# Kernel tuning notes

Hardware: AMD Instinct MI355X
Metric: run time of the kernel (lower is better)

## Reference

```python
import jax, jax.numpy as jnp
import numpy as np

D, H, L = 88, 256, 128  # input_dim, hidden_dim, latent_dim
B, T = 128, 1024


def setup_inputs() -> dict:
    key = jax.random.key(0)
    ks = jax.random.split(key, 16)
    s = 1.0 / np.sqrt(H)
    u = lambda k, shape: jax.random.uniform(k, shape, jnp.float32, -s, s)
    return {
        "x": jax.random.uniform(ks[0], (B, T, D), jnp.float32),  # piano-roll in [0,1)
        "Wih_e": u(ks[1], (4 * H, D)),
        "Whh_e": u(ks[2], (4 * H, H)),
        "bih_e": u(ks[3], (4 * H,)),
        "bhh_e": u(ks[4], (4 * H,)),
        "Wih_d": u(ks[5], (4 * H, D)),
        "Whh_d": u(ks[6], (4 * H, H)),
        "bih_d": u(ks[7], (4 * H,)),
        "bhh_d": u(ks[8], (4 * H,)),
        "W_lat": u(ks[9], (L, H)),
        "b_lat": u(ks[10], (L,)),
        "W_decinit": u(ks[11], (H, L)),
        "b_decinit": u(ks[12], (H,)),
        "W_out": u(ks[13], (D, H)),
        "b_out": u(ks[14], (D,)),
    }


def _lstm_cell(x_t, h, c, Wih, Whh, b):
    # PyTorch gate order: i, f, g, o
    gates = x_t @ Wih.T + h @ Whh.T + b  # [B, 4H]
    i, f, g, o = jnp.split(gates, 4, axis=-1)
    c_new = jax.nn.sigmoid(f) * c + jax.nn.sigmoid(i) * jnp.tanh(g)
    h_new = jax.nn.sigmoid(o) * jnp.tanh(c_new)
    return h_new, c_new


def reference(x, Wih_e, Whh_e, bih_e, bhh_e, Wih_d, Whh_d, bih_d, bhh_d,
              W_lat, b_lat, W_decinit, b_decinit, W_out, b_out):
    batch, seq_len, _ = x.shape
    b_e = bih_e + bhh_e
    b_d = bih_d + bhh_d

    # ---- encoder LSTM: scan over time, keep final hidden state ----
    def enc_step(carry, x_t):
        h, c = carry
        h, c = _lstm_cell(x_t, h, c, Wih_e, Whh_e, b_e)
        return (h, c), None

    h0 = jnp.zeros((batch, H), x.dtype)
    (h_n, _), _ = jax.lax.scan(enc_step, (h0, h0), jnp.swapaxes(x, 0, 1))

    # ---- latent + decoder init ----
    z = h_n @ W_lat.T + b_lat                     # [B, L]
    h_dec0 = z @ W_decinit.T + b_decinit          # [B, H]
    c_dec0 = jnp.zeros_like(h_dec0)
    inp0 = jnp.zeros((batch, D), x.dtype)

    def dec_step(carry, _):
        h, c, inp = carry
        h, c = _lstm_cell(inp, h, c, Wih_d, Whh_d, b_d)
        pred = jax.nn.sigmoid(h @ W_out.T + b_out)  # [B, D]
        return (h, c, pred), pred

    _, preds = jax.lax.scan(dec_step, (h_dec0, c_dec0, inp0), None, length=seq_len)
    outputs = jnp.swapaxes(preds, 0, 1)           # [B, T, D]
    return outputs, z
```

## Files before the change

kernel.cpp:

```cpp
#include <hip/hip_runtime.h>


typedef unsigned int u32;
typedef unsigned long long u64;
typedef unsigned short u16;

typedef _Float16 v8h __attribute__((ext_vector_type(8)));
typedef float    v4f __attribute__((ext_vector_type(4)));
typedef u32      v4u __attribute__((ext_vector_type(4)));

union H8 { v8h v; u64 q[2]; v4u u4; u32 d[4]; _Float16 h[8]; u16 s[8]; };

#define ENC_TAG(t) (0x4000u + (u32)(t))
#define DEC_TAG(t) (0x4800u + (u32)(t))
#define XW_OFF_U32   65536ull
#define XW_U32_PER_G 786432ull
#define WS_NEED ((XW_OFF_U32 + 8ull*XW_U32_PER_G) * 4ull)

static __device__ __forceinline__ float fsig(float x){
  return __builtin_amdgcn_rcpf(1.f + __builtin_amdgcn_exp2f(-1.4426950408889634f*x));
}
static __device__ __forceinline__ float ftanh(float x){
  return 1.f - 2.f*__builtin_amdgcn_rcpf(1.f + __builtin_amdgcn_exp2f(2.8853900817779268f*x));
}
static __device__ __forceinline__ u32 f2tag(float f, u32 tag){
  union{ _Float16 h; u16 b; } u; u.h = (_Float16)f;
  return (tag << 16) | (u32)u.b;
}

static __device__ __forceinline__ void st_pk4(u32* p, v4u val){
  asm volatile("global_store_dwordx4 %0, %1, off sc0 sc1" :: "v"(p), "v"(val) : "memory");
}
static __device__ __forceinline__ void poll_issue(const u32* p, v4u& q){
  asm volatile("global_load_dwordx4 %0, %1, off sc0 sc1" : "=v"(q) : "v"(p) : "memory");
}
static __device__ __forceinline__ void poll_sc01(const u32* p, v4u& q){
  asm volatile("global_load_dwordx4 %0, %1, off sc0 sc1\n\ts_waitcnt vmcnt(0)"
               : "=v"(q) : "v"(p) : "memory");
}
static __device__ __forceinline__ void poll_wait(v4u& q){
  asm volatile("s_waitcnt vmcnt(0)" : "+v"(q) :: "memory");
}

static __device__ __forceinline__ void poll_finish(const u32* p, u32 tag, v4u& q,
                                                   _Float16* dstbuf, int rbase, int scol){
  const u32 tm = tag << 16;
  poll_wait(q);
  u32 it = 0;
  for(;;){
    u32 bad = (q[0]^tm)|(q[1]^tm)|(q[2]^tm)|(q[3]^tm);
    if (__all((bad & 0xFFFF0000u) == 0)) break;
    if ((++it & 15u) == 0u) __builtin_amdgcn_s_sleep(1);
    poll_sc01(p, q);
  }
  #pragma unroll
  for (int j = 0; j < 4; ++j){
    const int row = rbase + j;
    const int ab = (row*512 + scol*2) ^ ((row&7)<<4);
    *(u16*)((char*)dstbuf + ab) = (u16)(q[j] & 0xFFFFu);
  }
}

static __device__ __forceinline__ v4u frag_h(const _Float16* b, int row, int colh){
  const int a = (row*512 + colh*2) ^ ((row&7)<<4);
  return *(const v4u*)((const char*)b + a);
}
static __device__ __forceinline__ v4u frag_x(const _Float16* b, int row, int colh){
  const int a = (row*256 + colh*2) ^ ((row&7)<<4);
  return *(const v4u*)((const char*)b + a);
}

static __device__ __forceinline__ void build_Bw(v8h Bw[4][11], const float* Wih,
                                                const float* Whh, int wcol, int quad, int hf){
  #pragma unroll
  for (int nt = 0; nt < 4; ++nt){
    const int n = nt*256 + wcol;
    #pragma unroll
    for (int kt = 0; kt < 11; ++kt){
      H8 a;
      #pragma unroll
      for (int j = 0; j < 8; ++j){
        float val;
        if (kt < 3){
          const int k = kt*32 + quad*8 + j;
          val = (k < 88) ? Wih[n*88 + k] : 0.f;
        } else {
          const int base = (kt < 7) ? (hf*128 + (kt-3)*32) : ((1-hf)*128 + (kt-7)*32);
          val = Whh[n*256 + base + quad*8 + j];
        }
        a.h[j] = (_Float16)val;
      }
      Bw[nt][kt] = a.v;
    }
  }
}

template<bool XW>
static __device__ __forceinline__ void load_Ax(H8 Ax[3], const float* x, const u32* xwg,
                                               int g, int t, int c, int quad, int l){
  if constexpr (XW){
    const u32* xb = xwg + (u64)t*768ull;
    #pragma unroll
    for (int kt = 0; kt < 3; ++kt)
      Ax[kt].u4 = *(const v4u*)(xb + kt*256 + l*4);
  } else {
    const float* xb = x + ((u64)(g*16 + c)*1024ull + (u64)t)*88ull;
    #pragma unroll
    for (int kt = 0; kt < 3; ++kt){
      if (kt == 2 && quad == 3){ Ax[kt].q[0] = 0; Ax[kt].q[1] = 0; }
      else {
        const int k0 = kt*32 + quad*8;
        v4f f0 = *(const v4f*)(xb + k0);
        v4f f1 = *(const v4f*)(xb + k0 + 4);
        #pragma unroll
        for (int j = 0; j < 4; ++j){ Ax[kt].h[j] = (_Float16)f0[j]; Ax[kt].h[j+4] = (_Float16)f1[j]; }
      }
    }
  }
}

static __device__ __forceinline__ void emit_h(const v4f acc[4], const float bb[4], float cst[4],
                                              _Float16* dstbuf, u32* hx_slot, u32 tag,
                                              int c, int quad, int wcol){
  v4u pk;
  #pragma unroll
  for (int r = 0; r < 4; ++r){
    const float gi = acc[0][r] + bb[0];
    const float gf = acc[1][r] + bb[1];
    const float gg = acc[2][r] + bb[2];
    const float go = acc[3][r] + bb[3];
    const float cn = fsig(gf)*cst[r] + fsig(gi)*ftanh(gg);
    cst[r] = cn;
    const float hn = fsig(go)*ftanh(cn);
    const int row = quad*4 + r;
    const int ab = (row*512 + wcol*2) ^ ((row&7)<<4);
    *(_Float16*)((char*)dstbuf + ab) = (_Float16)hn;
    pk[r] = f2tag(hn, tag);
  }
  st_pk4(hx_slot + ((wcol & 127)*16 + quad*4), pk);
}

__global__ __launch_bounds__(256) void xconv(const float* __restrict__ x, u32* __restrict__ xw){
  const int flat = (int)blockIdx.x*256 + (int)threadIdx.x;
  const int l  = flat & 63;
  const int f2 = flat >> 6;
  const int kt = f2 % 3;
  const int f3 = f2 / 3;
  const int t  = f3 & 1023;
  const int g  = f3 >> 10;
  const int c = l & 15, quad = l >> 4;
  H8 a;
  if (kt == 2 && quad == 3){ a.q[0] = 0; a.q[1] = 0; }
  else {
    const float* xb = x + ((u64)(g*16 + c)*1024ull + (u64)t)*88ull + kt*32 + quad*8;
    v4f f0 = *(const v4f*)xb;
    v4f f1 = *(const v4f*)(xb + 4);
    #pragma unroll
    for (int j = 0; j < 4; ++j){ a.h[j] = (_Float16)f0[j]; a.h[j+4] = (_Float16)f1[j]; }
  }
  *(v4u*)(xw + (u64)flat*4ull) = a.u4;
}

template<bool XW>
__global__ __launch_bounds__(512, 2) void lstm_ae(
    const float* __restrict__ x,
    const float* __restrict__ Wih_e, const float* __restrict__ Whh_e,
    const float* __restrict__ bih_e, const float* __restrict__ bhh_e,
    const float* __restrict__ Wih_d, const float* __restrict__ Whh_d,
    const float* __restrict__ bih_d, const float* __restrict__ bhh_d,
    const float* __restrict__ W_lat, const float* __restrict__ b_lat,
    const float* __restrict__ W_decinit, const float* __restrict__ b_decinit,
    const float* __restrict__ W_out, const float* __restrict__ b_out,
    float* __restrict__ dout, char* __restrict__ ws)
{
  const int tid = (int)threadIdx.x;
  const int v = tid >> 6, l = tid & 63;
  const int c = l & 15, quad = l >> 4;
  const int bid = (int)blockIdx.x;
  const int g = bid & 7, hf = bid >> 3;
  const int wcol = hf*128 + v*16 + c;
  const int kL = hf*4;
  const int kR = 4 - hf*4;

  u32* wsu = (u32*)ws;
  u32* hx_w       = wsu + (u64)((g*2 + hf)*2)     * 2048ull;
  const u32* hx_r = wsu + (u64)((g*2 + (1-hf))*2) * 2048ull;
  const u32* xwg  = wsu + XW_OFF_U32 + (u64)g * XW_U32_PER_G;

  const int rbase = (tid & 3) * 4;
  const int scol  = (1-hf)*128 + (tid >> 2);

  __shared__ _Float16 h2[2][4096];
  __shared__ _Float16 xp[2048];
  __shared__ v4u woutlds[3072];

  #pragma unroll
  for (int i = 0; i < 6; ++i){
    const int fid = v*6 + i;
    const int nt = fid >> 3, kt = fid & 7;
    const int n = nt*16 + c, k0 = kt*32 + quad*8;
    H8 a;
    #pragma unroll
    for (int j = 0; j < 8; ++j)
      a.h[j] = (n < 88) ? (_Float16)W_out[n*256 + k0 + j] : (_Float16)0.f;
    woutlds[fid*64 + l] = a.u4;
  }

  v8h Bw[4][11];
  build_Bw(Bw, Wih_e, Whh_e, wcol, quad, hf);
  float bb[4];
  #pragma unroll
  for (int nt = 0; nt < 4; ++nt) bb[nt] = bih_e[nt*256 + wcol] + bhh_e[nt*256 + wcol];
  float cst[4] = {0.f, 0.f, 0.f, 0.f};
  __syncthreads();

  {
    H8 Ax[3];
    load_Ax<XW>(Ax, x, xwg, g, 0, c, quad, l);
    v4f acc[4];
    #pragma unroll
    for (int nt = 0; nt < 4; ++nt) acc[nt] = (v4f){0.f,0.f,0.f,0.f};
    #pragma unroll
    for (int kt = 0; kt < 3; ++kt)
      #pragma unroll
      for (int nt = 0; nt < 4; ++nt)
        acc[nt] = __builtin_amdgcn_mfma_f32_16x16x32_f16(Ax[kt].v, Bw[nt][kt], acc[nt], 0,0,0);
    emit_h(acc, bb, cst, h2[0], hx_w, ENC_TAG(0), c, quad, wcol);
    __syncthreads();
  }

  v4f accx[4];
  {
    H8 Ax[3];
    load_Ax<XW>(Ax, x, xwg, g, 1, c, quad, l);
    #pragma unroll
    for (int nt = 0; nt < 4; ++nt) accx[nt] = (v4f){0.f,0.f,0.f,0.f};
    #pragma unroll
    for (int kt = 0; kt < 3; ++kt)
      #pragma unroll
      for (int nt = 0; nt < 4; ++nt)
        accx[nt] = __builtin_amdgcn_mfma_f32_16x16x32_f16(Ax[kt].v, Bw[nt][kt], accx[nt], 0,0,0);
  }

  #pragma unroll 1
  for (int t = 1; t < 1024; ++t){
    const int cur = (t-1)&1, nxt = t&1;
    const u32* pp = hx_r + (u64)cur*2048ull + tid*4;
    v4u q; poll_issue(pp, q);

    v4f acc[4];
    #pragma unroll
    for (int nt = 0; nt < 4; ++nt) acc[nt] = accx[nt];

    H8 AhL[4];
    #pragma unroll
    for (int i = 0; i < 4; ++i) AhL[i].u4 = frag_h(h2[cur], c, (kL+i)*32 + quad*8);
    #pragma unroll
    for (int i = 0; i < 4; ++i)
      #pragma unroll
      for (int nt = 0; nt < 4; ++nt)
        acc[nt] = __builtin_amdgcn_mfma_f32_16x16x32_f16(AhL[i].v, Bw[nt][3+i], acc[nt], 0,0,0);

    if (t < 1023){
      H8 Ax[3];
      load_Ax<XW>(Ax, x, xwg, g, t+1, c, quad, l);
      #pragma unroll
      for (int nt = 0; nt < 4; ++nt) accx[nt] = (v4f){0.f,0.f,0.f,0.f};
      #pragma unroll
      for (int kt = 0; kt < 3; ++kt)
        #pragma unroll
        for (int nt = 0; nt < 4; ++nt)
          accx[nt] = __builtin_amdgcn_mfma_f32_16x16x32_f16(Ax[kt].v, Bw[nt][kt], accx[nt], 0,0,0);
    }

    poll_finish(pp, ENC_TAG(t-1), q, h2[cur], rbase, scol);
    __syncthreads();

    H8 AhR[4];
    #pragma unroll
    for (int i = 0; i < 4; ++i) AhR[i].u4 = frag_h(h2[cur], c, (kR+i)*32 + quad*8);
    #pragma unroll
    for (int i = 0; i < 4; ++i)
      #pragma unroll
      for (int nt = 0; nt < 4; ++nt)
        acc[nt] = __builtin_amdgcn_mfma_f32_16x16x32_f16(AhR[i].v, Bw[nt][7+i], acc[nt], 0,0,0);

    emit_h(acc, bb, cst, h2[nxt], hx_w + (u64)nxt*2048ull, ENC_TAG(t), c, quad, wcol);
    __syncthreads();
  }

  {
    const u32* pp = hx_r + 2048ull + tid*4;
    v4u q; poll_issue(pp, q);
    poll_finish(pp, ENC_TAG(1023), q, h2[1], rbase, scol);
    __syncthreads();
  }

  {
    H8 AhL[4], AhR[4];
    #pragma unroll
    for (int i = 0; i < 4; ++i) AhL[i].u4 = frag_h(h2[1], c, (kL+i)*32 + quad*8);
    #pragma unroll
    for (int i = 0; i < 4; ++i) AhR[i].u4 = frag_h(h2[1], c, (kR+i)*32 + quad*8);
    const int n = v*16 + c;
    v4f zacc = (v4f){0.f,0.f,0.f,0.f};
    #pragma unroll
    for (int i = 0; i < 4; ++i){
      H8 b; const int k0 = (kL+i)*32 + quad*8;
      #pragma unroll
      for (int j = 0; j < 8; ++j) b.h[j] = (_Float16)W_lat[n*256 + k0 + j];
      zacc = __builtin_amdgcn_mfma_f32_16x16x32_f16(AhL[i].v, b.v, zacc, 0,0,0);
    }
    #pragma unroll
    for (int i = 0; i < 4; ++i){
      H8 b; const int k0 = (kR+i)*32 + quad*8;
      #pragma unroll
      for (int j = 0; j < 8; ++j) b.h[j] = (_Float16)W_lat[n*256 + k0 + j];
      zacc = __builtin_amdgcn_mfma_f32_16x16x32_f16(AhR[i].v, b.v, zacc, 0,0,0);
    }
    const float bl = b_lat[n];
    #pragma unroll
    for (int r = 0; r < 4; ++r){
      const int m = quad*4 + r;
      const float zv = zacc[r] + bl;
      if (hf == 0)
        __builtin_nontemporal_store(zv, dout + 11534336ull + (u64)(g*16 + m)*128ull + n);
      const int ab = (m*256 + n*2) ^ ((m&7)<<4);
      *(_Float16*)((char*)xp + ab) = (_Float16)zv;
    }
    __syncthreads();
  }

  {
    H8 Az[4];
    #pragma unroll
    for (int kt = 0; kt < 4; ++kt) Az[kt].u4 = frag_x(xp, c, kt*32 + quad*8);
    #pragma unroll
    for (int half = 0; half < 2; ++half){
      const int n = half*128 + v*16 + c;
      v4f da = (v4f){0.f,0.f,0.f,0.f};
      #pragma unroll
      for (int kt = 0; kt < 4; ++kt){
        H8 b; const int k0 = kt*32 + quad*8;
        #pragma unroll
        for (int j = 0; j < 8; ++j) b.h[j] = (_Float16)W_decinit[n*128 + k0 + j];
        da = __builtin_amdgcn_mfma_f32_16x16x32_f16(Az[kt].v, b.v, da, 0,0,0);
      }
      const float bdi = b_decinit[n];
      #pragma unroll
      for (int r = 0; r < 4; ++r){
        const int row = quad*4 + r;
        const int ab = (row*512 + n*2) ^ ((row&7)<<4);
        *(_Float16*)((char*)h2[1] + ab) = (_Float16)(da[r] + bdi);
      }
    }
    __syncthreads();
  }

  build_Bw(Bw, Wih_d, Whh_d, wcol, quad, hf);
  #pragma unroll
  for (int nt = 0; nt < 4; ++nt) bb[nt] = bih_d[nt*256 + wcol] + bhh_d[nt*256 + wcol];
  float bo = 0.f;
  if (v < 6){ const int n = v*16 + c; bo = (n < 88) ? b_out[n] : 0.f; }
  #pragma unroll
  for (int r = 0; r < 4; ++r) cst[r] = 0.f;

  #pragma unroll 1
  for (int t = 0; t < 1024; ++t){
    const int cur = (t+1)&1, nxt = t&1;
    const u32* pp = hx_r + (u64)cur*2048ull + tid*4;
    v4u q;
    if (t > 0) poll_issue(pp, q);

    H8 AhL[4], AhR[4];
    v4f acc[4];
    #pragma unroll
    for (int nt = 0; nt < 4; ++nt) acc[nt] = (v4f){0.f,0.f,0.f,0.f};
    #pragma unroll
    for (int i = 0; i < 4; ++i) AhL[i].u4 = frag_h(h2[cur], c, (kL+i)*32 + quad*8);
    #pragma unroll
    for (int i = 0; i < 4; ++i)
      #pragma unroll
      for (int nt = 0; nt < 4; ++nt)
        acc[nt] = __builtin_amdgcn_mfma_f32_16x16x32_f16(AhL[i].v, Bw[nt][3+i], acc[nt], 0,0,0);

    v4f pacc = (v4f){0.f,0.f,0.f,0.f};
    if (t > 0 && v < 6){
      #pragma unroll
      for (int i = 0; i < 4; ++i){
        H8 b; b.u4 = woutlds[(v*8 + kL + i)*64 + l];
        pacc = __builtin_amdgcn_mfma_f32_16x16x32_f16(AhL[i].v, b.v, pacc, 0,0,0);
      }
    }

    if (t > 0) poll_finish(pp, DEC_TAG(t-1), q, h2[cur], rbase, scol);
    __syncthreads();

    #pragma unroll
    for (int i = 0; i < 4; ++i) AhR[i].u4 = frag_h(h2[cur], c, (kR+i)*32 + quad*8);
    #pragma unroll
    for (int i = 0; i < 4; ++i)
      #pragma unroll
      for (int nt = 0; nt < 4; ++nt)
        acc[nt] = __builtin_amdgcn_mfma_f32_16x16x32_f16(AhR[i].v, Bw[nt][7+i], acc[nt], 0,0,0);

    if (t > 0 && v < 6){
      #pragma unroll
      for (int i = 0; i < 4; ++i){
        H8 b; b.u4 = woutlds[(v*8 + kR + i)*64 + l];
        pacc = __builtin_amdgcn_mfma_f32_16x16x32_f16(AhR[i].v, b.v, pacc, 0,0,0);
      }
      const int n = v*16 + c;
      #pragma unroll
      for (int r = 0; r < 4; ++r){
        const float pv = fsig(pacc[r] + bo);
        const int m = quad*4 + r;
        const int ab = (m*256 + n*2) ^ ((m&7)<<4);
        *(_Float16*)((char*)xp + ab) = (_Float16)pv;
        if (hf == 0 && n < 88)
          __builtin_nontemporal_store(pv,
            dout + ((u64)(g*16 + m)*1024ull + (u64)(t-1))*88ull + n);
      }
    }
    __syncthreads();

    if (t > 0){
      H8 Ap[3];
      #pragma unroll
      for (int kt = 0; kt < 3; ++kt) Ap[kt].u4 = frag_x(xp, c, kt*32 + quad*8);
      #pragma unroll
      for (int kt = 0; kt < 3; ++kt)
        #pragma unroll
        for (int nt = 0; nt < 4; ++nt)
          acc[nt] = __builtin_amdgcn_mfma_f32_16x16x32_f16(Ap[kt].v, Bw[nt][kt], acc[nt], 0,0,0);
    }

    emit_h(acc, bb, cst, h2[nxt], hx_w + (u64)nxt*2048ull, DEC_TAG(t), c, quad, wcol);
    __syncthreads();
  }

  {
    const u32* pp = hx_r + 2048ull + tid*4;
    v4u q; poll_issue(pp, q);
    poll_finish(pp, DEC_TAG(1023), q, h2[1], rbase, scol);
    __syncthreads();
    if (hf == 0 && v < 6){
      const int n = v*16 + c;
      v4f pacc = (v4f){0.f,0.f,0.f,0.f};
      #pragma unroll
      for (int i = 0; i < 4; ++i){
        H8 a; a.u4 = frag_h(h2[1], c, (kL+i)*32 + quad*8);
        H8 b; b.u4 = woutlds[(v*8 + kL + i)*64 + l];
        pacc = __builtin_amdgcn_mfma_f32_16x16x32_f16(a.v, b.v, pacc, 0,0,0);
      }
      #pragma unroll
      for (int i = 0; i < 4; ++i){
        H8 a; a.u4 = frag_h(h2[1], c, (kR+i)*32 + quad*8);
        H8 b; b.u4 = woutlds[(v*8 + kR + i)*64 + l];
        pacc = __builtin_amdgcn_mfma_f32_16x16x32_f16(a.v, b.v, pacc, 0,0,0);
      }
      if (n < 88){
        #pragma unroll
        for (int r = 0; r < 4; ++r){
          const float pv = fsig(pacc[r] + bo);
          const int m = quad*4 + r;
          __builtin_nontemporal_store(pv,
            dout + ((u64)(g*16 + m)*1024ull + 1023ull)*88ull + n);
        }
      }
    }
  }
}

extern "C" void kernel_launch(void* const* d_in, const int* in_sizes, int n_in,
                              void* d_out, int out_size, void* d_ws, size_t ws_size,
                              hipStream_t stream){
  (void)in_sizes; (void)n_in; (void)out_size;
  const bool xw_ok = ws_size >= WS_NEED;
  if (xw_ok){
    hipLaunchKernelGGL(xconv, dim3(6144), dim3(256), 0, stream,
                       (const float*)d_in[0], (u32*)d_ws + XW_OFF_U32);
    hipLaunchKernelGGL((lstm_ae<true>), dim3(16), dim3(512), 0, stream,
      (const float*)d_in[0],  (const float*)d_in[1],  (const float*)d_in[2],
      (const float*)d_in[3],  (const float*)d_in[4],  (const float*)d_in[5],
      (const float*)d_in[6],  (const float*)d_in[7],  (const float*)d_in[8],
      (const float*)d_in[9],  (const float*)d_in[10], (const float*)d_in[11],
      (const float*)d_in[12], (const float*)d_in[13], (const float*)d_in[14],
      (float*)d_out, (char*)d_ws);
  } else {
    hipLaunchKernelGGL((lstm_ae<false>), dim3(16), dim3(512), 0, stream,
      (const float*)d_in[0],  (const float*)d_in[1],  (const float*)d_in[2],
      (const float*)d_in[3],  (const float*)d_in[4],  (const float*)d_in[5],
      (const float*)d_in[6],  (const float*)d_in[7],  (const float*)d_in[8],
      (const float*)d_in[9],  (const float*)d_in[10], (const float*)d_in[11],
      (const float*)d_in[12], (const float*)d_in[13], (const float*)d_in[14],
      (float*)d_out, (char*)d_ws);
  }
}
```

Baseline: 6.191 ms.

## Pair LSTM blocks by XCC and poll same-die partners with lighter cache scope

Each of the 16 blocks reads its XCC ID and publishes it to a control area that xconv zeroes. The blocks then agree on a pairing in which the two halves of a batch group run on the same XCC whenever possible. Paired blocks on the same die poll the exchanged hidden state with sc0-only loads, mostly skipping sc1, which is meant to cut the per-step cross-block handshake latency in both recurrences. This adds a startup rendezvous that assumes all 16 blocks are co-resident, and it relies on the L2 being coherent within an XCC.

```diff
diff --git a/kernel.cpp b/kernel.cpp
--- a/kernel.cpp
+++ b/kernel.cpp
@@ -15,7 +15,8 @@
 #define DEC_TAG(t) (0x4800u + (u32)(t))
 #define XW_OFF_U32   65536ull
 #define XW_U32_PER_G 786432ull
-#define WS_NEED ((XW_OFF_U32 + 8ull*XW_U32_PER_G) * 4ull)
+#define CTRL_OFF_U32 (XW_OFF_U32 + 8ull*XW_U32_PER_G)
+#define WS_NEED ((CTRL_OFF_U32 + 64ull) * 4ull)
 
 static __device__ __forceinline__ float fsig(float x){
   return __builtin_amdgcn_rcpf(1.f + __builtin_amdgcn_exp2f(-1.4426950408889634f*x));
@@ -31,10 +32,15 @@
 static __device__ __forceinline__ void st_pk4(u32* p, v4u val){
   asm volatile("global_store_dwordx4 %0, %1, off sc0 sc1" :: "v"(p), "v"(val) : "memory");
 }
-static __device__ __forceinline__ void poll_issue(const u32* p, v4u& q){
-  asm volatile("global_load_dwordx4 %0, %1, off sc0 sc1" : "=v"(q) : "v"(p) : "memory");
-}
-static __device__ __forceinline__ void poll_sc01(const u32* p, v4u& q){
+static __device__ __forceinline__ void poll_issue(const u32* p, v4u& q, bool same){
+  if (same) asm volatile("global_load_dwordx4 %0, %1, off sc0" : "=v"(q) : "v"(p) : "memory");
+  else      asm volatile("global_load_dwordx4 %0, %1, off sc0 sc1" : "=v"(q) : "v"(p) : "memory");
+}
+static __device__ __forceinline__ void poll_fast(const u32* p, v4u& q){
+  asm volatile("global_load_dwordx4 %0, %1, off sc0\n\ts_waitcnt vmcnt(0)"
+               : "=v"(q) : "v"(p) : "memory");
+}
+static __device__ __forceinline__ void poll_mall(const u32* p, v4u& q){
   asm volatile("global_load_dwordx4 %0, %1, off sc0 sc1\n\ts_waitcnt vmcnt(0)"
                : "=v"(q) : "v"(p) : "memory");
 }
@@ -43,15 +49,18 @@
 }
 
 static __device__ __forceinline__ void poll_finish(const u32* p, u32 tag, v4u& q,
-                                                   _Float16* dstbuf, int rbase, int scol){
+                                                   _Float16* dstbuf, int rbase, int scol,
+                                                   bool same){
   const u32 tm = tag << 16;
   poll_wait(q);
   u32 it = 0;
   for(;;){
     u32 bad = (q[0]^tm)|(q[1]^tm)|(q[2]^tm)|(q[3]^tm);
     if (__all((bad & 0xFFFF0000u) == 0)) break;
-    if ((++it & 15u) == 0u) __builtin_amdgcn_s_sleep(1);
-    poll_sc01(p, q);
+    ++it;
+    if ((it & 15u) == 0u) __builtin_amdgcn_s_sleep(1);
+    if (same && (it & 3u) != 0u) poll_fast(p, q);
+    else                         poll_mall(p, q);
   }
   #pragma unroll
   for (int j = 0; j < 4; ++j){
@@ -140,7 +149,11 @@
   st_pk4(hx_slot + ((wcol & 127)*16 + quad*4), pk);
 }
 
-__global__ __launch_bounds__(256) void xconv(const float* __restrict__ x, u32* __restrict__ xw){
+__global__ __launch_bounds__(256) void xconv(const float* __restrict__ x, u32* __restrict__ wsu){
+  if (blockIdx.x == 0 && threadIdx.x < 64)
+    __hip_atomic_store(&wsu[CTRL_OFF_U32 + threadIdx.x], 0u,
+                       __ATOMIC_RELAXED, __HIP_MEMORY_SCOPE_AGENT);
+  u32* xw = wsu + XW_OFF_U32;
   const int flat = (int)blockIdx.x*256 + (int)threadIdx.x;
   const int l  = flat & 63;
   const int f2 = flat >> 6;
@@ -177,12 +190,65 @@
   const int v = tid >> 6, l = tid & 63;
   const int c = l & 15, quad = l >> 4;
   const int bid = (int)blockIdx.x;
-  const int g = bid & 7, hf = bid >> 3;
+
+  u32* wsu = (u32*)ws;
+
+  __shared__ int pinfo[3];
+  if constexpr (XW){
+    if (tid == 0){
+      u32 xcc;
+      asm volatile("s_getreg_b32 %0, hwreg(HW_REG_XCC_ID)" : "=s"(xcc));
+      xcc &= 15u;
+      u32* ctrl = wsu + CTRL_OFF_U32;
+      __hip_atomic_store(&ctrl[8+bid], xcc + 1u, __ATOMIC_RELEASE, __HIP_MEMORY_SCOPE_AGENT);
+      int xs[16];
+      #pragma unroll 1
+      for(;;){
+        bool all = true;
+        #pragma unroll 1
+        for (int i = 0; i < 16; ++i){
+          const u32 vi = __hip_atomic_load(&ctrl[8+i], __ATOMIC_ACQUIRE, __HIP_MEMORY_SCOPE_AGENT);
+          xs[i] = (int)vi - 1;
+          all = all && (vi != 0u);
+        }
+        if (all) break;
+        __builtin_amdgcn_s_sleep(2);
+      }
+      int G = -1, HF = 0, SM = 0, pc = 0;
+      int lo[16]; int nl = 0;
+      #pragma unroll 1
+      for (int xc = 0; xc < 16; ++xc){
+        int prev = -1;
+        #pragma unroll 1
+        for (int i = 0; i < 16; ++i) if (xs[i] == xc){
+          if (prev < 0) prev = i;
+          else {
+            if (prev == bid){ G = pc; HF = 0; SM = 1; }
+            if (i    == bid){ G = pc; HF = 1; SM = 1; }
+            ++pc; prev = -1;
+          }
+        }
+        if (prev >= 0) lo[nl++] = prev;
+      }
+      #pragma unroll 1
+      for (int j = 0; j + 1 < nl; j += 2){
+        if (lo[j]   == bid){ G = pc; HF = 0; SM = 0; }
+        if (lo[j+1] == bid){ G = pc; HF = 1; SM = 0; }
+        ++pc;
+      }
+      if (G < 0){ G = bid & 7; HF = bid >> 3; SM = 0; }
+      pinfo[0] = G; pinfo[1] = HF; pinfo[2] = SM;
+    }
+    __syncthreads();
+  }
+  const int g    = XW ? pinfo[0] : (bid & 7);
+  const int hf   = XW ? pinfo[1] : (bid >> 3);
+  const bool same = XW ? (pinfo[2] != 0) : false;
+
   const int wcol = hf*128 + v*16 + c;
   const int kL = hf*4;
   const int kR = 4 - hf*4;
 
-  u32* wsu = (u32*)ws;
   u32* hx_w       = wsu + (u64)((g*2 + hf)*2)     * 2048ull;
   const u32* hx_r = wsu + (u64)((g*2 + (1-hf))*2) * 2048ull;
   const u32* xwg  = wsu + XW_OFF_U32 + (u64)g * XW_U32_PER_G;
@@ -246,7 +312,7 @@
   for (int t = 1; t < 1024; ++t){
     const int cur = (t-1)&1, nxt = t&1;
     const u32* pp = hx_r + (u64)cur*2048ull + tid*4;
-    v4u q; poll_issue(pp, q);
+    v4u q; poll_issue(pp, q, same);
 
     v4f acc[4];
     #pragma unroll
@@ -273,7 +339,7 @@
           accx[nt] = __builtin_amdgcn_mfma_f32_16x16x32_f16(Ax[kt].v, Bw[nt][kt], accx[nt], 0,0,0);
     }
 
-    poll_finish(pp, ENC_TAG(t-1), q, h2[cur], rbase, scol);
+    poll_finish(pp, ENC_TAG(t-1), q, h2[cur], rbase, scol, same);
     __syncthreads();
 
     H8 AhR[4];
@@ -291,8 +357,8 @@
 
   {
     const u32* pp = hx_r + 2048ull + tid*4;
-    v4u q; poll_issue(pp, q);
-    poll_finish(pp, ENC_TAG(1023), q, h2[1], rbase, scol);
+    v4u q; poll_issue(pp, q, same);
+    poll_finish(pp, ENC_TAG(1023), q, h2[1], rbase, scol, same);
     __syncthreads();
   }
 
@@ -370,7 +436,7 @@
     const int cur = (t+1)&1, nxt = t&1;
     const u32* pp = hx_r + (u64)cur*2048ull + tid*4;
     v4u q;
-    if (t > 0) poll_issue(pp, q);
+    if (t > 0) poll_issue(pp, q, same);
 
     H8 AhL[4], AhR[4];
     v4f acc[4];
@@ -393,7 +459,7 @@
       }
     }
 
-    if (t > 0) poll_finish(pp, DEC_TAG(t-1), q, h2[cur], rbase, scol);
+    if (t > 0) poll_finish(pp, DEC_TAG(t-1), q, h2[cur], rbase, scol, same);
     __syncthreads();
 
     #pragma unroll
@@ -441,8 +507,8 @@
 
   {
     const u32* pp = hx_r + 2048ull + tid*4;
-    v4u q; poll_issue(pp, q);
-    poll_finish(pp, DEC_TAG(1023), q, h2[1], rbase, scol);
+    v4u q; poll_issue(pp, q, same);
+    poll_finish(pp, DEC_TAG(1023), q, h2[1], rbase, scol, same);
     __syncthreads();
     if (hf == 0 && v < 6){
       const int n = v*16 + c;
@@ -479,7 +545,7 @@
   const bool xw_ok = ws_size >= WS_NEED;
   if (xw_ok){
     hipLaunchKernelGGL(xconv, dim3(6144), dim3(256), 0, stream,
-                       (const float*)d_in[0], (u32*)d_ws + XW_OFF_U32);
+                       (const float*)d_in[0], (u32*)d_ws);
     hipLaunchKernelGGL((lstm_ae<true>), dim3(16), dim3(512), 0, stream,
       (const float*)d_in[0],  (const float*)d_in[1],  (const float*)d_in[2],
       (const float*)d_in[3],  (const float*)d_in[4],  (const float*)d_in[5],
```

Result: slower. 7.102 ms (+14.7%).
